# Kernel optimization log

Measured on AMD Instinct MI355X. Metric: run time of the kernel, lower is better.

Reference implementation:

```python
import jax, jax.numpy as jnp
import numpy as np

D = 768; NH = 12; DH = 64; DEPTH = 12; P = 16; IMG = 224; NC = 1000; DFF = 3072
GAMMA = 0.01; MIN_TOKENS = 16; EPS = 1e-6
SCALE = DH ** -0.5
NPATCH = (IMG // P) ** 2  # 196


def _ln(x, w, b, eps=1e-6):
    mu = x.mean(-1, keepdims=True)
    var = ((x - mu) ** 2).mean(-1, keepdims=True)
    return (x - mu) * jax.lax.rsqrt(var + eps) * w + b


def _block(x, p):
    # one pre-norm ViT block; returns new x, attention matrix A [B,H,T,T], values v [B,H,T,DH]
    (l1w, l1b, qw, qb, pw, pb, l2w, l2b, f1w, f1b, f2w, f2b) = p
    B, T, _ = x.shape
    qkv = _ln(x, l1w, l1b) @ qw + qb                      # [B,T,3D]
    qkv = qkv.reshape(B, T, 3, NH, DH).transpose(2, 0, 3, 1, 4)
    q, k, v = qkv[0], qkv[1], qkv[2]                      # [B,H,T,DH]
    A = jax.nn.softmax(jnp.einsum('bhtd,bhsd->bhts', q, k) * SCALE, axis=-1)
    out = jnp.einsum('bhts,bhsd->bhtd', A, v).transpose(0, 2, 1, 3).reshape(B, T, NH * DH)
    x = x + out @ pw + pb
    h = jax.nn.gelu(_ln(x, l2w, l2b) @ f1w + f1b, approximate=False)
    x = x + h @ f2w + f2b
    return x, A, v


def _embed(x, patch_w, patch_b, cls_token, pos_embed):
    B = x.shape[0]
    feat = jax.lax.conv_general_dilated(x, patch_w, (P, P), 'VALID',
                                        dimension_numbers=('NCHW', 'OIHW', 'NCHW'))  # [B,D,14,14]
    feat = feat.reshape(B, D, -1).transpose(0, 2, 1) + patch_b                       # [B,196,D]
    cls = jnp.broadcast_to(cls_token, (B, 1, D))
    return jnp.concatenate([cls, feat], axis=1) + pos_embed                          # [B,197,D]


def setup_inputs() -> dict:
    key = jax.random.key(0)
    ks = jax.random.split(key, 12)
    s = 0.02
    n = lambda k, shape: jax.random.normal(k, shape, jnp.float32) * s
    return {
        'x': jax.random.normal(ks[0], (32, 3, IMG, IMG), jnp.float32),
        'patch_w': n(ks[1], (D, 3, P, P)),
        'patch_b': jnp.zeros((D,), jnp.float32),
        'cls_token': n(ks[2], (1, 1, D)),
        'pos_embed': n(ks[3], (1, NPATCH + 1, D)),
        'ln1_w': jnp.ones((DEPTH, D), jnp.float32),
        'ln1_b': jnp.zeros((DEPTH, D), jnp.float32),
        'qkv_w': n(ks[4], (DEPTH, D, 3 * D)),
        'qkv_b': jnp.zeros((DEPTH, 3 * D), jnp.float32),
        'proj_w': n(ks[5], (DEPTH, D, D)),
        'proj_b': jnp.zeros((DEPTH, D), jnp.float32),
        'ln2_w': jnp.ones((DEPTH, D), jnp.float32),
        'ln2_b': jnp.zeros((DEPTH, D), jnp.float32),
        'fc1_w': n(ks[6], (DEPTH, D, DFF)),
        'fc1_b': jnp.zeros((DEPTH, DFF), jnp.float32),
        'fc2_w': n(ks[7], (DEPTH, DFF, D)),
        'fc2_b': jnp.zeros((DEPTH, D), jnp.float32),
        'norm_w': jnp.ones((D,), jnp.float32),
        'norm_b': jnp.zeros((D,), jnp.float32),
        'head_w': n(ks[8], (D, NC)),
        'head_b': jnp.zeros((NC,), jnp.float32),
    }


def reference(x, patch_w, patch_b, cls_token, pos_embed, ln1_w, ln1_b, qkv_w, qkv_b,
              proj_w, proj_b, ln2_w, ln2_b, fc1_w, fc1_b, fc2_w, fc2_b,
              norm_w, norm_b, head_w, head_b):
    # NOTE: token pruning produces data-dependent shapes, so this runs eagerly
    # (Python control flow on concrete values), exactly mirroring the torch code.
    x = _embed(x, patch_w, patch_b, cls_token, pos_embed)
    N = x.shape[1] - 1
    prev_mass = None
    for l in range(DEPTH):
        p = (ln1_w[l], ln1_b[l], qkv_w[l], qkv_b[l], proj_w[l], proj_b[l],
             ln2_w[l], ln2_b[l], fc1_w[l], fc1_b[l], fc2_w[l], fc2_b[l])
        x, A, v = _block(x, p)
        if N <= MIN_TOKENS:
            continue
        Am = A.mean(axis=1)                                   # [B,T,T] head-mean attention
        Vm = v.mean(axis=1)                                   # [B,T,DH] head-mean values
        rho = (1.0 + Am[:, 0, 0] * jnp.linalg.norm(Vm[:, 0], axis=-1)).mean()
        A_cls = Am[:, 0, 1:N + 1]                             # [B,N] cls->patch attention
        V_pt = Vm[:, 1:N + 1]
        Vc = V_pt - V_pt.mean(axis=1, keepdims=True)
        Vn = jnp.linalg.norm(Vc, axis=-1)                     # [B,N]
        mu = Vn.mean(axis=1, keepdims=True)
        sd = Vn.std(axis=1, keepdims=True, ddof=1)            # torch.std is unbiased
        J = A_cls * jax.nn.relu((Vn - mu) / (sd + EPS))       # [B,N] Jacobian score
        mass = J.sum(axis=1).mean()
        if prev_mass is not None:
            eta = mass / (prev_mass + EPS)
            keep_ratio = jnp.clip(rho * eta, 0.25, 4.0) ** (-GAMMA)
            N_next = max(MIN_TOKENS, int(N * float(keep_ratio)))
        else:
            N_next = N
        if N_next < N:
            idx = jnp.sort(jax.lax.top_k(J.mean(axis=0), N_next)[1]) + 1
            keep = jnp.concatenate([jnp.zeros((1,), idx.dtype), idx])
            x = x[:, keep]
            N = N_next
        prev_mass = mass
    x = _ln(x, norm_w, norm_b)
    return x[:, 0] @ head_w + head_b
```

## Files before the change

kernel.cpp:

```cpp
#include <hip/hip_runtime.h>
#include <math.h>

#define D 768
#define NH 12
#define DH 64
#define DEPTH 12
#define TMAX 197
#define NPATCH 196
#define BATCH 32
#define DFF 3072
#define NC 1000
#define QSTRIDE 2304
#define SCALE 0.125f
#define EPSF 1e-6f

typedef __bf16 bf16x8 __attribute__((ext_vector_type(8)));
typedef float f32x4 __attribute__((ext_vector_type(4)));
typedef short sshort8 __attribute__((ext_vector_type(8)));


__device__ __forceinline__ short f2bf(float x) {
  unsigned u = __float_as_uint(x);
  u = u + 0x7fffu + ((u >> 16) & 1u);
  return (short)(u >> 16);
}
__device__ __forceinline__ float bf2f(short h) {
  return __uint_as_float(((unsigned)(unsigned short)h) << 16);
}
__device__ __forceinline__ void bsplit(float x, short* hp, short* lp) {
  short h = f2bf(x);
  *hp = h;
  *lp = f2bf(x - bf2f(h));
}

__device__ __forceinline__ void gll16(const void* g, void* l) {
  __builtin_amdgcn_global_load_lds(
      (const __attribute__((address_space(1))) void*)g,
      (__attribute__((address_space(3))) void*)l, 16, 0, 0);
}


__device__ __forceinline__ float block_reduce_sum(float v, float* red, int tid) {
  red[tid] = v; __syncthreads();
  #pragma unroll
  for (int o = 128; o > 0; o >>= 1) { if (tid < o) red[tid] += red[tid + o]; __syncthreads(); }
  float r = red[0]; __syncthreads();
  return r;
}

__global__ void fail_kernel(float* out) { out[0] = 1.0e6f; }

__global__ void init_kernel(int* si, float* sf) {
  si[0] = TMAX;
  si[1] = 0;
  si[2] = 0;
  sf[0] = 0.f;
}

__global__ void wsplit_t(const float* __restrict__ W, short* __restrict__ Wpk,
                         int K, int N) {
  __shared__ float t[32][33];
  int n0 = blockIdx.x * 32, k0 = blockIdx.y * 32;
  int tid = threadIdx.x;
  int kk = tid >> 3, n4 = (tid & 7) * 4;
  float4 v = *(const float4*)(W + (size_t)(k0 + kk) * N + n0 + n4);
  t[kk][n4] = v.x; t[kk][n4 + 1] = v.y; t[kk][n4 + 2] = v.z; t[kk][n4 + 3] = v.w;
  __syncthreads();
  int nn = tid >> 3, k4 = (tid & 7) * 4;
  short* dh = Wpk + (size_t)(n0 + nn) * 2 * K + k0 + k4;
  short* dl = dh + K;
  #pragma unroll
  for (int c = 0; c < 4; ++c) bsplit(t[k4 + c][nn], &dh[c], &dl[c]);
}

__global__ void wsplit_nt(const float* __restrict__ W, short* __restrict__ Wpk, int K) {
  const float* src = W + (size_t)blockIdx.x * K;
  short* dh = Wpk + (size_t)blockIdx.x * 2 * K;
  short* dl = dh + K;
  for (int k = threadIdx.x; k < K; k += 256) bsplit(src[k], &dh[k], &dl[k]);
}


__global__ void im2col_kernel(const float* __restrict__ x, short* __restrict__ Impk) {
  int p = blockIdx.x, b = blockIdx.y;
  int py = p / 14, px = p % 14;
  short* dst = Impk + ((size_t)b * NPATCH + p) * 1536;
  for (int k = threadIdx.x; k < D; k += 256) {
    int c = k >> 8; int rem = k & 255; int i = rem >> 4; int j = rem & 15;
    float v = x[(((size_t)b * 3 + c) * 224 + py * 16 + i) * 224 + px * 16 + j];
    bsplit(v, &dst[k], &dst[768 + k]);
  }
}

__global__ void assemble_kernel(const float* __restrict__ PE, const float* __restrict__ cls,
                                const float* __restrict__ pos, float* __restrict__ X) {
  int t = blockIdx.x, b = blockIdx.y; int tid = threadIdx.x;
  float* xp = X + ((size_t)(b * TMAX) + t) * D;
  for (int k = tid; k < D; k += 256) {
    float v = (t == 0) ? cls[k] : PE[((size_t)(b * NPATCH) + (t - 1)) * D + k];
    xp[k] = v + pos[(size_t)t * D + k];
  }
}


__global__ void ln_kernel(const float* __restrict__ Xin, short* __restrict__ XNpk,
                          const float* __restrict__ wgt, const float* __restrict__ bsh,
                          const int* __restrict__ si) {
  int row = blockIdx.x;
  if ((row % TMAX) >= si[0]) return;
  __shared__ float red[256];
  int tid = threadIdx.x;
  const float* xp = Xin + (size_t)row * D;
  float v0 = xp[tid], v1 = xp[tid + 256], v2 = xp[tid + 512];
  float mu = block_reduce_sum(v0 + v1 + v2, red, tid) * (1.0f / 768.0f);
  float d0 = v0 - mu, d1 = v1 - mu, d2 = v2 - mu;
  float var = block_reduce_sum(d0 * d0 + d1 * d1 + d2 * d2, red, tid) * (1.0f / 768.0f);
  float inv = 1.0f / sqrtf(var + EPSF);
  short* op = XNpk + (size_t)row * 1536;
  float y0 = d0 * inv * wgt[tid] + bsh[tid];
  float y1 = d1 * inv * wgt[tid + 256] + bsh[tid + 256];
  float y2 = d2 * inv * wgt[tid + 512] + bsh[tid + 512];
  bsplit(y0, &op[tid], &op[768 + tid]);
  bsplit(y1, &op[tid + 256], &op[768 + tid + 256]);
  bsplit(y2, &op[tid + 512], &op[768 + tid + 512]);
}

__global__ void lnfinal_kernel(const float* __restrict__ X, float* __restrict__ CLSb,
                               const float* __restrict__ wgt, const float* __restrict__ bsh) {
  int b = blockIdx.x; int tid = threadIdx.x;
  __shared__ float red[256];
  const float* xp = X + (size_t)b * TMAX * D;
  float v0 = xp[tid], v1 = xp[tid + 256], v2 = xp[tid + 512];
  float mu = block_reduce_sum(v0 + v1 + v2, red, tid) * (1.0f / 768.0f);
  float d0 = v0 - mu, d1 = v1 - mu, d2 = v2 - mu;
  float var = block_reduce_sum(d0 * d0 + d1 * d1 + d2 * d2, red, tid) * (1.0f / 768.0f);
  float inv = 1.0f / sqrtf(var + EPSF);
  float* op = CLSb + (size_t)b * D;
  op[tid]       = d0 * inv * wgt[tid]       + bsh[tid];
  op[tid + 256] = d1 * inv * wgt[tid + 256] + bsh[tid + 256];
  op[tid + 512] = d2 * inv * wgt[tid + 512] + bsh[tid + 512];
}


#define GTM 128
#define GTN 128
#define GTK 32

template<int EPI>
__global__ __launch_bounds__(256)
void mgemm_kernel(const short* __restrict__ Apk, const short* __restrict__ Bpk,
                  const float* __restrict__ bias, const float* __restrict__ Rsrc,
                  float* __restrict__ Cf, short* __restrict__ Cpk,
                  int M, int K, int N) {
  __shared__ char lds[65536];
  const int tid = threadIdx.x;
  const int ln = tid & 63;
  const int wv = tid >> 6;
  const int wm = wv >> 1, wn = wv & 1;
  const int m0 = blockIdx.y * GTM, n0 = blockIdx.x * GTN;
  const int lm = ln & 15, kc = ln >> 4;
  const size_t rs = 2 * (size_t)K;

  f32x4 acc[4][4];
  f32x4 zv = {0.f, 0.f, 0.f, 0.f};
  #pragma unroll
  for (int i = 0; i < 4; ++i)
    #pragma unroll
    for (int j = 0; j < 4; ++j) acc[i][j] = zv;

  auto stage = [&](int k0, int buf) {
    char* base = lds + (buf << 15);
    #pragma unroll
    for (int i = 0; i < 4; ++i) {
      int s = (i << 8) + tid;
      int r = s >> 3;
      int sl = (s & 7) ^ (r & 7);
      size_t eoff = (size_t)(sl >> 2) * K + (size_t)(k0 + ((sl & 3) << 3));
      int ldsoff = ((i << 8) + (tid & 192)) << 4;
      gll16(Apk + (size_t)(m0 + r) * rs + eoff, base + ldsoff);
      gll16(Bpk + (size_t)(n0 + r) * rs + eoff, base + 16384 + ldsoff);
    }
  };

  const int nk = K / GTK;
  stage(0, 0);
  for (int kt = 0; kt < nk; ++kt) {
    __syncthreads();
    if (kt + 1 < nk) stage((kt + 1) * GTK, (kt + 1) & 1);
    const char* pa = lds + ((kt & 1) << 15);
    const char* pb = pa + 16384;
    bf16x8 bh[4], bl[4];
    #pragma unroll
    for (int j = 0; j < 4; ++j) {
      int c = wn * 64 + j * 16 + lm;
      int bo = c * 128 + ((kc ^ (c & 7)) << 4);
      bh[j] = *(const bf16x8*)(pb + bo);
      bl[j] = *(const bf16x8*)(pb + (bo ^ 64));
    }
    #pragma unroll
    for (int i = 0; i < 4; ++i) {
      int r = wm * 64 + i * 16 + lm;
      int ao = r * 128 + ((kc ^ (r & 7)) << 4);
      bf16x8 ah = *(const bf16x8*)(pa + ao);
      bf16x8 al = *(const bf16x8*)(pa + (ao ^ 64));
      #pragma unroll
      for (int j = 0; j < 4; ++j) {
        acc[i][j] = __builtin_amdgcn_mfma_f32_16x16x32_bf16(ah, bh[j], acc[i][j], 0, 0, 0);
        acc[i][j] = __builtin_amdgcn_mfma_f32_16x16x32_bf16(ah, bl[j], acc[i][j], 0, 0, 0);
        acc[i][j] = __builtin_amdgcn_mfma_f32_16x16x32_bf16(al, bh[j], acc[i][j], 0, 0, 0);
      }
    }
  }

  #pragma unroll
  for (int i = 0; i < 4; ++i) {
    #pragma unroll
    for (int t = 0; t < 4; ++t) {
      int m = m0 + wm * 64 + i * 16 + kc * 4 + t;
      if (m >= M) continue;
      #pragma unroll
      for (int j = 0; j < 4; ++j) {
        int n = n0 + wn * 64 + j * 16 + lm;
        float v = acc[i][j][t] + bias[n];
        if (EPI == 1) v += Rsrc[(size_t)m * N + n];
        if (EPI == 2) {
          v = v * 0.5f * (1.0f + erff(v * 0.70710678118654752f));
          short h = f2bf(v);
          Cpk[(size_t)m * 2 * N + n] = h;
          Cpk[(size_t)m * 2 * N + N + n] = f2bf(v - bf2f(h));
        } else {
          Cf[(size_t)m * N + n] = v;
        }
      }
    }
  }
}


#define BM 128
#define BN 64
#define BK 16

__global__ __launch_bounds__(256, 2)
void gemm_kernel(const float* __restrict__ A, const float* __restrict__ Bw,
                 const float* __restrict__ bias, float* __restrict__ C,
                 int M, int K, int N) {
  __shared__ float As[BK][BM + 4];
  __shared__ float Bs[BK][BN];
  int tid = threadIdx.x;
  int tx = tid & 15;
  int ty = tid >> 4;
  int m0 = blockIdx.y * BM;
  int n0 = blockIdx.x * BN;
  float acc[8][4];
  #pragma unroll
  for (int i = 0; i < 8; ++i)
    #pragma unroll
    for (int j = 0; j < 4; ++j) acc[i][j] = 0.f;
  const int lkA = tid & 15;
  const int lmA = tid >> 4;
  const int lnB = tid & 63;
  const int lkB = tid >> 6;
  for (int k0 = 0; k0 < K; k0 += BK) {
    #pragma unroll
    for (int r = 0; r < 8; ++r) {
      int ml = r * 16 + lmA;
      int m = m0 + ml;
      float va = 0.f;
      if (m < M) va = A[(size_t)m * K + k0 + lkA];
      As[lkA][ml] = va;
    }
    #pragma unroll
    for (int r = 0; r < 4; ++r) {
      int kk = r * 4 + lkB;
      int n = n0 + lnB;
      float vb = 0.f;
      if (n < N) vb = Bw[(size_t)(k0 + kk) * N + n];
      Bs[kk][lnB] = vb;
    }
    __syncthreads();
    #pragma unroll
    for (int kk = 0; kk < BK; ++kk) {
      const float4 b4 = *(const float4*)(&Bs[kk][tx * 4]);
      const float4 a0 = *(const float4*)(&As[kk][ty * 8]);
      const float4 a1 = *(const float4*)(&As[kk][ty * 8 + 4]);
      const float a[8] = {a0.x, a0.y, a0.z, a0.w, a1.x, a1.y, a1.z, a1.w};
      const float bb[4] = {b4.x, b4.y, b4.z, b4.w};
      #pragma unroll
      for (int i = 0; i < 8; ++i)
        #pragma unroll
        for (int j = 0; j < 4; ++j)
          acc[i][j] = fmaf(a[i], bb[j], acc[i][j]);
    }
    __syncthreads();
  }
  #pragma unroll
  for (int i = 0; i < 8; ++i) {
    int m = m0 + ty * 8 + i;
    if (m >= M) continue;
    #pragma unroll
    for (int j = 0; j < 4; ++j) {
      int n = n0 + tx * 4 + j;
      if (n >= N) continue;
      C[(size_t)m * N + n] = acc[i][j] + bias[n];
    }
  }
}


#define QT 64
#define KVT 64

__global__ __launch_bounds__(256)
void mattn_kernel(const float* __restrict__ QKV, short* __restrict__ AOpk,
                  const int* __restrict__ si) {
  const int tok = si[0];
  const int bh = blockIdx.x; const int b = bh / NH, h = bh % NH;
  const int q0 = blockIdx.y * QT;
  if (q0 >= tok) return;
  __shared__ short Kh[4096], Kl[4096], Vth[4096], Vtl[4096];
  __shared__ short Pb[8192];
  const int tid = threadIdx.x;
  const int l = tid & 63, w = tid >> 6;
  const int lm = l & 15, lg = l >> 4;

  bf16x8 qh[2], ql[2];
  {
    int qrow = q0 + w * 16 + lm;
    if (qrow >= TMAX) qrow = TMAX - 1;
    const float* qp = QKV + (size_t)(b * TMAX + qrow) * QSTRIDE + h * DH + lg * 8;
    #pragma unroll
    for (int c = 0; c < 2; ++c) {
      sshort8 hs, ls;
      #pragma unroll
      for (int j = 0; j < 8; ++j) {
        float v = qp[c * 32 + j];
        short hh = f2bf(v);
        hs[j] = hh;
        ls[j] = f2bf(v - bf2f(hh));
      }
      qh[c] = __builtin_bit_cast(bf16x8, hs);
      ql[c] = __builtin_bit_cast(bf16x8, ls);
    }
  }

  float mrun[4], lrun[4];
  f32x4 oacc[4];
  f32x4 zv = {0.f, 0.f, 0.f, 0.f};
  #pragma unroll
  for (int t = 0; t < 4; ++t) { mrun[t] = -1e30f; lrun[t] = 0.f; }
  #pragma unroll
  for (int j = 0; j < 4; ++j) oacc[j] = zv;

  const int r0 = (tid >> 4) * 4;
  const int td4 = (tid & 15) * 4;

  for (int j0 = 0; j0 < tok; j0 += KVT) {
    {
      float vbuf[16];
      #pragma unroll
      for (int i = 0; i < 4; ++i) {
        int gr = j0 + r0 + i; if (gr >= TMAX) gr = TMAX - 1;
        const float* kp = QKV + (size_t)(b * TMAX + gr) * QSTRIDE + D + h * DH + td4;
        float4 kv = *(const float4*)kp;
        short4 sh, sl;
        sh.x = f2bf(kv.x); sl.x = f2bf(kv.x - bf2f(sh.x));
        sh.y = f2bf(kv.y); sl.y = f2bf(kv.y - bf2f(sh.y));
        sh.z = f2bf(kv.z); sl.z = f2bf(kv.z - bf2f(sh.z));
        sh.w = f2bf(kv.w); sl.w = f2bf(kv.w - bf2f(sh.w));
        int r = r0 + i;
        int so = r * 64 + (((td4 >> 3) ^ (r & 7)) << 3) + (td4 & 7);
        *(short4*)(Kh + so) = sh;
        *(short4*)(Kl + so) = sl;
        const float* vp = QKV + (size_t)(b * TMAX + gr) * QSTRIDE + 2 * D + h * DH + td4;
        float4 vv = *(const float4*)vp;
        vbuf[i * 4 + 0] = vv.x; vbuf[i * 4 + 1] = vv.y;
        vbuf[i * 4 + 2] = vv.z; vbuf[i * 4 + 3] = vv.w;
      }
      #pragma unroll
      for (int dd = 0; dd < 4; ++dd) {
        int d = td4 + dd;
        short4 sh, sl;
        float c0 = vbuf[dd], c1 = vbuf[4 + dd], c2 = vbuf[8 + dd], c3 = vbuf[12 + dd];
        sh.x = f2bf(c0); sl.x = f2bf(c0 - bf2f(sh.x));
        sh.y = f2bf(c1); sl.y = f2bf(c1 - bf2f(sh.y));
        sh.z = f2bf(c2); sl.z = f2bf(c2 - bf2f(sh.z));
        sh.w = f2bf(c3); sl.w = f2bf(c3 - bf2f(sh.w));
        int so = d * 64 + (((r0 >> 3) ^ (d & 7)) << 3) + (r0 & 7);
        *(short4*)(Vth + so) = sh;
        *(short4*)(Vtl + so) = sl;
      }
    }
    __syncthreads();

    f32x4 sacc[4];
    #pragma unroll
    for (int jk = 0; jk < 4; ++jk) sacc[jk] = zv;
    #pragma unroll
    for (int c = 0; c < 2; ++c) {
      #pragma unroll
      for (int jk = 0; jk < 4; ++jk) {
        int row = jk * 16 + lm;
        int so = row * 64 + (((c * 4 + lg) ^ (row & 7)) << 3);
        bf16x8 kbh = *(const bf16x8*)(Kh + so);
        bf16x8 kbl = *(const bf16x8*)(Kl + so);
        sacc[jk] = __builtin_amdgcn_mfma_f32_16x16x32_bf16(qh[c], kbh, sacc[jk], 0, 0, 0);
        sacc[jk] = __builtin_amdgcn_mfma_f32_16x16x32_bf16(qh[c], kbl, sacc[jk], 0, 0, 0);
        sacc[jk] = __builtin_amdgcn_mfma_f32_16x16x32_bf16(ql[c], kbh, sacc[jk], 0, 0, 0);
      }
    }

    float p[4][4];
    #pragma unroll
    for (int jk = 0; jk < 4; ++jk) {
      bool valid = (j0 + jk * 16 + lm) < tok;
      #pragma unroll
      for (int t = 0; t < 4; ++t)
        p[jk][t] = valid ? sacc[jk][t] * SCALE : -1e30f;
    }
    float mt[4], mnew[4], co[4], rs[4];
    #pragma unroll
    for (int t = 0; t < 4; ++t) {
      mt[t] = fmaxf(fmaxf(p[0][t], p[1][t]), fmaxf(p[2][t], p[3][t]));
      #pragma unroll
      for (int off = 1; off < 16; off <<= 1)
        mt[t] = fmaxf(mt[t], __shfl_xor(mt[t], off, 16));
      mnew[t] = fmaxf(mrun[t], mt[t]);
      co[t] = expf(mrun[t] - mnew[t]);
      rs[t] = 0.f;
    }
    #pragma unroll
    for (int jk = 0; jk < 4; ++jk)
      #pragma unroll
      for (int t = 0; t < 4; ++t) {
        p[jk][t] = expf(p[jk][t] - mnew[t]);
        rs[t] += p[jk][t];
      }
    #pragma unroll
    for (int t = 0; t < 4; ++t) {
      #pragma unroll
      for (int off = 1; off < 16; off <<= 1)
        rs[t] += __shfl_xor(rs[t], off, 16);
      lrun[t] = lrun[t] * co[t] + rs[t];
      mrun[t] = mnew[t];
    }
    #pragma unroll
    for (int jd = 0; jd < 4; ++jd)
      #pragma unroll
      for (int t = 0; t < 4; ++t) oacc[jd][t] *= co[t];

    short* Pw = Pb + w * 2048;
    #pragma unroll
    for (int jk = 0; jk < 4; ++jk)
      #pragma unroll
      for (int t = 0; t < 4; ++t) {
        int q = lg * 4 + t;
        int col = jk * 16 + lm;
        short hh = f2bf(p[jk][t]);
        short hl = f2bf(p[jk][t] - bf2f(hh));
        int so = q * 64 + (((col >> 3) ^ (q & 7)) << 3) + (col & 7);
        Pw[so] = hh;
        Pw[1024 + so] = hl;
      }

    #pragma unroll
    for (int c = 0; c < 2; ++c) {
      int aro = lm * 64 + (((c * 4 + lg) ^ (lm & 7)) << 3);
      bf16x8 pah = *(const bf16x8*)(Pw + aro);
      bf16x8 pal = *(const bf16x8*)(Pw + 1024 + aro);
      #pragma unroll
      for (int jd = 0; jd < 4; ++jd) {
        int d = jd * 16 + lm;
        int so = d * 64 + (((c * 4 + lg) ^ (d & 7)) << 3);
        bf16x8 vbh = *(const bf16x8*)(Vth + so);
        bf16x8 vbl = *(const bf16x8*)(Vtl + so);
        oacc[jd] = __builtin_amdgcn_mfma_f32_16x16x32_bf16(pah, vbh, oacc[jd], 0, 0, 0);
        oacc[jd] = __builtin_amdgcn_mfma_f32_16x16x32_bf16(pah, vbl, oacc[jd], 0, 0, 0);
        oacc[jd] = __builtin_amdgcn_mfma_f32_16x16x32_bf16(pal, vbh, oacc[jd], 0, 0, 0);
      }
    }
    __syncthreads();
  }

  #pragma unroll
  for (int t = 0; t < 4; ++t) {
    int q = q0 + w * 16 + lg * 4 + t;
    if (q >= tok) continue;
    float inv = 1.0f / lrun[t];
    short* op = AOpk + (size_t)(b * TMAX + q) * 1536 + h * DH;
    #pragma unroll
    for (int jd = 0; jd < 4; ++jd) {
      int d = jd * 16 + lm;
      float y = oacc[jd][t] * inv;
      short hh = f2bf(y);
      op[d] = hh;
      op[768 + d] = f2bf(y - bf2f(hh));
    }
  }
}

__global__ void clsrow_kernel(const float* __restrict__ QKV, float* __restrict__ Pcls,
                              const int* __restrict__ si) {
  int tok = si[0];
  int bh = blockIdx.x; int b = bh / NH, h = bh % NH;
  int tid = threadIdx.x;
  __shared__ float q[DH];
  __shared__ float red[256];
  if (tid < DH) q[tid] = QKV[((size_t)(b * TMAX)) * QSTRIDE + h * DH + tid];
  __syncthreads();
  float sval = -1e30f;
  if (tid < tok) {
    const float* kp = QKV + ((size_t)(b * TMAX) + tid) * QSTRIDE + D + h * DH;
    float a = 0.f;
    #pragma unroll
    for (int dd = 0; dd < DH; ++dd) a = fmaf(q[dd], kp[dd], a);
    sval = a * SCALE;
  }
  red[tid] = sval; __syncthreads();
  #pragma unroll
  for (int o = 128; o > 0; o >>= 1) { if (tid < o) red[tid] = fmaxf(red[tid], red[tid + o]); __syncthreads(); }
  float mx = red[0]; __syncthreads();
  float e = (tid < tok) ? expf(sval - mx) : 0.f;
  red[tid] = e; __syncthreads();
  #pragma unroll
  for (int o = 128; o > 0; o >>= 1) { if (tid < o) red[tid] += red[tid + o]; __syncthreads(); }
  if (tid < tok) Pcls[(size_t)bh * TMAX + tid] = e / red[0];
}

__global__ void aclsmean_kernel(const float* __restrict__ Pcls, float* __restrict__ Acls,
                                const int* __restrict__ si) {
  int tok = si[0]; int b = blockIdx.x; int tid = threadIdx.x;
  if (tid < tok) {
    float s = 0.f;
    #pragma unroll
    for (int h = 0; h < NH; ++h) s += Pcls[((size_t)b * NH + h) * TMAX + tid];
    Acls[b * TMAX + tid] = s * (1.0f / 12.0f);
  }
}

__global__ void vmean_kernel(const float* __restrict__ QKV, float* __restrict__ Vm,
                             const int* __restrict__ si) {
  int tok = si[0];
  int t = blockIdx.x, b = blockIdx.y;
  if (t >= tok) return;
  int d = threadIdx.x;
  const float* vp = QKV + ((size_t)(b * TMAX + t)) * QSTRIDE + 2 * D;
  float s = 0.f;
  #pragma unroll
  for (int h = 0; h < NH; ++h) s += vp[h * DH + d];
  Vm[((size_t)b * TMAX + t) * DH + d] = s * (1.0f / 12.0f);
}


__global__ void stats_kernel(const float* __restrict__ Vm, const float* __restrict__ Acls,
                             float* __restrict__ Jbuf, float* __restrict__ Jsum,
                             float* __restrict__ rhot, const int* __restrict__ si) {
  int tok = si[0]; int N = tok - 1;
  if (N <= 16) return;
  int b = blockIdx.x; int tid = threadIdx.x;
  __shared__ float red[256];
  __shared__ float vmean[DH];
  __shared__ float Vn[NPATCH];
  const float* vb = Vm + (size_t)b * TMAX * DH;

  float x0 = 0.f;
  if (tid < DH) { float v = vb[tid]; x0 = v * v; }
  red[tid] = x0; __syncthreads();
  #pragma unroll
  for (int o = 128; o > 0; o >>= 1) { if (tid < o) red[tid] += red[tid + o]; __syncthreads(); }
  if (tid == 0) rhot[b] = 1.0f + Acls[b * TMAX] * sqrtf(red[0]);
  __syncthreads();

  int d = tid & 63, part = tid >> 6;
  float s = 0.f;
  for (int t = 1 + part; t <= N; t += 4) s += vb[(size_t)t * DH + d];
  red[tid] = s; __syncthreads();
  if (tid < DH) vmean[tid] = (red[tid] + red[tid + 64] + red[tid + 128] + red[tid + 192]) / (float)N;
  __syncthreads();

  if (tid < N) {
    const float* vp = vb + (size_t)(tid + 1) * DH;
    float a = 0.f;
    #pragma unroll
    for (int dd = 0; dd < DH; ++dd) { float z = vp[dd] - vmean[dd]; a = fmaf(z, z, a); }
    Vn[tid] = sqrtf(a);
  }
  __syncthreads();

  red[tid] = (tid < N) ? Vn[tid] : 0.f; __syncthreads();
  #pragma unroll
  for (int o = 128; o > 0; o >>= 1) { if (tid < o) red[tid] += red[tid + o]; __syncthreads(); }
  float mu = red[0] / (float)N;
  __syncthreads();
  float dv = (tid < N) ? (Vn[tid] - mu) : 0.f;
  red[tid] = dv * dv; __syncthreads();
  #pragma unroll
  for (int o = 128; o > 0; o >>= 1) { if (tid < o) red[tid] += red[tid + o]; __syncthreads(); }
  float sd = sqrtf(red[0] / (float)(N - 1));
  __syncthreads();

  float Jv = 0.f;
  if (tid < N) {
    float z = (Vn[tid] - mu) / (sd + EPSF);
    z = fmaxf(z, 0.f);
    Jv = Acls[b * TMAX + 1 + tid] * z;
    Jbuf[b * NPATCH + tid] = Jv;
  }
  red[tid] = Jv; __syncthreads();
  #pragma unroll
  for (int o = 128; o > 0; o >>= 1) { if (tid < o) red[tid] += red[tid + o]; __syncthreads(); }
  if (tid == 0) Jsum[b] = red[0];
}

__global__ void decide_kernel(const float* __restrict__ Jbuf, const float* __restrict__ Jsum,
                              const float* __restrict__ rhot, int* __restrict__ keep,
                              int* __restrict__ si, float* __restrict__ sf) {
  int tok = si[0]; int N = tok - 1;
  int tid = threadIdx.x;
  if (N <= 16) { if (tid == 0) si[2] = 0; return; }
  __shared__ float red[256];
  __shared__ float Jms[NPATCH];
  __shared__ int sel[NPATCH];

  red[tid] = (tid < BATCH) ? rhot[tid] : 0.f; __syncthreads();
  #pragma unroll
  for (int o = 128; o > 0; o >>= 1) { if (tid < o) red[tid] += red[tid + o]; __syncthreads(); }
  float rho = red[0] / (float)BATCH; __syncthreads();
  red[tid] = (tid < BATCH) ? Jsum[tid] : 0.f; __syncthreads();
  #pragma unroll
  for (int o = 128; o > 0; o >>= 1) { if (tid < o) red[tid] += red[tid + o]; __syncthreads(); }
  float mass = red[0] / (float)BATCH;
  int prev_valid = si[1];
  float prev = sf[0];
  __syncthreads();

  int N_next = N;
  if (prev_valid) {
    float eta = mass / (prev + EPSF);
    float re = rho * eta;
    re = fminf(fmaxf(re, 0.25f), 4.0f);
    double kr = pow((double)re, -0.01);
    int nn = (int)((double)N * kr);
    N_next = nn > 16 ? nn : 16;
  }
  if (tid == 0) { si[1] = 1; sf[0] = mass; }

  if (N_next < N) {
    if (tid < N) {
      float sJ = 0.f;
      for (int bb = 0; bb < BATCH; ++bb) sJ += Jbuf[bb * NPATCH + tid];
      Jms[tid] = sJ / (float)BATCH;
    }
    __syncthreads();
    if (tid < N) {
      float me = Jms[tid]; int rank = 0;
      for (int s2 = 0; s2 < N; ++s2) {
        float ov = Jms[s2];
        if (ov > me || (ov == me && s2 < tid)) ++rank;
      }
      sel[tid] = (rank < N_next) ? 1 : 0;
    }
    __syncthreads();
    if (tid == 0) {
      int c = 0; keep[c++] = 0;
      for (int t2 = 0; t2 < N; ++t2) if (sel[t2]) keep[c++] = t2 + 1;
      si[0] = N_next + 1;
      si[2] = 1;
    }
  } else {
    if (tid == 0) si[2] = 0;
  }
}

__global__ void gather_kernel(const float* __restrict__ X, float* __restrict__ T,
                              const int* __restrict__ keep, const int* __restrict__ si) {
  if (!si[2]) return;
  int tok = si[0];
  int i = blockIdx.x, b = blockIdx.y;
  if (i >= tok) return;
  int src = keep[i];
  const float* xp = X + ((size_t)(b * TMAX) + src) * D;
  float* tp = T + ((size_t)(b * TMAX) + i) * D;
  int tid = threadIdx.x;
  tp[tid] = xp[tid]; tp[tid + 256] = xp[tid + 256]; tp[tid + 512] = xp[tid + 512];
}

__global__ void copyback_kernel(const float* __restrict__ T, float* __restrict__ X,
                                const int* __restrict__ si) {
  if (!si[2]) return;
  int tok = si[0];
  int i = blockIdx.x, b = blockIdx.y;
  if (i >= tok) return;
  const float* tp = T + ((size_t)(b * TMAX) + i) * D;
  float* xp = X + ((size_t)(b * TMAX) + i) * D;
  int tid = threadIdx.x;
  xp[tid] = tp[tid]; xp[tid + 256] = tp[tid + 256]; xp[tid + 512] = tp[tid + 512];
}


extern "C" void kernel_launch(void* const* d_in, const int* in_sizes, int n_in,
                              void* d_out, int out_size, void* d_ws, size_t ws_size,
                              hipStream_t stream) {
  (void)in_sizes; (void)n_in; (void)out_size;
  const float* x       = (const float*)d_in[0];
  const float* patch_w = (const float*)d_in[1];
  const float* patch_b = (const float*)d_in[2];
  const float* cls_tok = (const float*)d_in[3];
  const float* pos     = (const float*)d_in[4];
  const float* ln1w    = (const float*)d_in[5];
  const float* ln1b    = (const float*)d_in[6];
  const float* qkvw    = (const float*)d_in[7];
  const float* qkvb    = (const float*)d_in[8];
  const float* projw   = (const float*)d_in[9];
  const float* projb   = (const float*)d_in[10];
  const float* ln2w    = (const float*)d_in[11];
  const float* ln2b    = (const float*)d_in[12];
  const float* fc1w    = (const float*)d_in[13];
  const float* fc1b    = (const float*)d_in[14];
  const float* fc2w    = (const float*)d_in[15];
  const float* fc2b    = (const float*)d_in[16];
  const float* normw   = (const float*)d_in[17];
  const float* normb   = (const float*)d_in[18];
  const float* headw   = (const float*)d_in[19];
  const float* headb   = (const float*)d_in[20];
  float* out = (float*)d_out;

  char* w = (char*)d_ws;
  size_t off = 0;
  auto alloc = [&](size_t bytes) -> void* {
    void* p = w + off;
    off += (bytes + 255) & ~(size_t)255;
    return p;
  };
  const size_t MROWS = (size_t)BATCH * TMAX;
  float* X    = (float*)alloc(MROWS * D * 4);
  short* XNpk = (short*)alloc(MROWS * 1536 * 2);
  float* QKV  = (float*)alloc(MROWS * QSTRIDE * 4);
  short* AOpk = (short*)alloc(MROWS * 1536 * 2);
  short* Hpk  = (short*)alloc(MROWS * 2 * DFF * 2);
  float* Vm   = (float*)alloc(MROWS * DH * 4);
  float* Pcls = (float*)alloc((size_t)BATCH * NH * TMAX * 4);
  float* Acls = (float*)alloc((size_t)BATCH * TMAX * 4);
  float* Jbuf = (float*)alloc((size_t)BATCH * NPATCH * 4);
  float* Jsum = (float*)alloc(BATCH * 4);
  float* rhot = (float*)alloc(BATCH * 4);
  int*   keep = (int*)alloc(256 * 4);
  int*   si   = (int*)alloc(64 * 4);
  float* sf   = (float*)alloc(64 * 4);
  float* CLS  = (float*)alloc((size_t)BATCH * D * 4);
  short* Wq   = (short*)alloc((size_t)QSTRIDE * 2 * D * 2);
  short* Wp   = (short*)alloc((size_t)D * 2 * D * 2);
  short* W1   = (short*)alloc((size_t)DFF * 2 * D * 2);
  short* W2   = (short*)alloc((size_t)D * 2 * DFF * 2);
  short* Wpat = (short*)alloc((size_t)D * 2 * D * 2);
  short* Impk = Hpk;
  float* TMP  = (float*)Hpk;
  float* Ef32 = QKV;

  if (off > ws_size) {
    fail_kernel<<<1, 1, 0, stream>>>(out);
    return;
  }

  init_kernel<<<1, 1, 0, stream>>>(si, sf);

  im2col_kernel<<<dim3(NPATCH, BATCH), 256, 0, stream>>>(x, Impk);
  wsplit_nt<<<D, 256, 0, stream>>>(patch_w, Wpat, D);
  mgemm_kernel<0><<<dim3(D / GTN, (BATCH * NPATCH + GTM - 1) / GTM), 256, 0, stream>>>(
      Impk, Wpat, patch_b, nullptr, Ef32, nullptr, BATCH * NPATCH, D, D);
  assemble_kernel<<<dim3(TMAX, BATCH), 256, 0, stream>>>(Ef32, cls_tok, pos, X);

  const int MG = (int)((MROWS + GTM - 1) / GTM);

  for (int l = 0; l < DEPTH; ++l) {
    const float* l1w = ln1w + l * D;
    const float* l1b = ln1b + l * D;
    const float* qw  = qkvw + (size_t)l * D * 3 * D;
    const float* qb  = qkvb + (size_t)l * 3 * D;
    const float* pw  = projw + (size_t)l * D * D;
    const float* pb  = projb + (size_t)l * D;
    const float* l2w = ln2w + l * D;
    const float* l2b = ln2b + l * D;
    const float* f1w = fc1w + (size_t)l * D * DFF;
    const float* f1b = fc1b + (size_t)l * DFF;
    const float* f2w = fc2w + (size_t)l * DFF * D;
    const float* f2b = fc2b + (size_t)l * D;

    wsplit_t<<<dim3(QSTRIDE / 32, D / 32), 256, 0, stream>>>(qw, Wq, D, QSTRIDE);
    wsplit_t<<<dim3(D / 32, D / 32), 256, 0, stream>>>(pw, Wp, D, D);
    wsplit_t<<<dim3(DFF / 32, D / 32), 256, 0, stream>>>(f1w, W1, D, DFF);
    wsplit_t<<<dim3(D / 32, DFF / 32), 256, 0, stream>>>(f2w, W2, DFF, D);

    ln_kernel<<<BATCH * TMAX, 256, 0, stream>>>(X, XNpk, l1w, l1b, si);
    mgemm_kernel<0><<<dim3(QSTRIDE / GTN, MG), 256, 0, stream>>>(
        XNpk, Wq, qb, nullptr, QKV, nullptr, (int)MROWS, D, QSTRIDE);
    mattn_kernel<<<dim3(BATCH * NH, (TMAX + QT - 1) / QT), 256, 0, stream>>>(QKV, AOpk, si);
    clsrow_kernel<<<BATCH * NH, 256, 0, stream>>>(QKV, Pcls, si);
    aclsmean_kernel<<<BATCH, 256, 0, stream>>>(Pcls, Acls, si);
    vmean_kernel<<<dim3(TMAX, BATCH), 64, 0, stream>>>(QKV, Vm, si);
    mgemm_kernel<1><<<dim3(D / GTN, MG), 256, 0, stream>>>(
        AOpk, Wp, pb, X, X, nullptr, (int)MROWS, D, D);
    ln_kernel<<<BATCH * TMAX, 256, 0, stream>>>(X, XNpk, l2w, l2b, si);
    mgemm_kernel<2><<<dim3(DFF / GTN, MG), 256, 0, stream>>>(
        XNpk, W1, f1b, nullptr, nullptr, Hpk, (int)MROWS, D, DFF);
    mgemm_kernel<1><<<dim3(D / GTN, MG), 256, 0, stream>>>(
        Hpk, W2, f2b, X, X, nullptr, (int)MROWS, DFF, D);
    stats_kernel<<<BATCH, 256, 0, stream>>>(Vm, Acls, Jbuf, Jsum, rhot, si);
    decide_kernel<<<1, 256, 0, stream>>>(Jbuf, Jsum, rhot, keep, si, sf);
    gather_kernel<<<dim3(TMAX, BATCH), 256, 0, stream>>>(X, TMP, keep, si);
    copyback_kernel<<<dim3(TMAX, BATCH), 256, 0, stream>>>(TMP, X, si);
  }

  lnfinal_kernel<<<BATCH, 256, 0, stream>>>(X, CLS, normw, normb);
  gemm_kernel<<<dim3(16, 1), 256, 0, stream>>>(CLS, headw, headb, out, BATCH, D, NC);
}
```

Before: 6.481 ms.

## Stage GEMM tiles through registers with single LDS buffer and swizzled block order

The GEMM kernel drops the double-buffered direct global-to-LDS loads. It now prefetches the next K-tile into registers while computing from a single 32KB LDS buffer, which halves LDS use so that three blocks can fit per CU (launch_bounds 256,3). The grid is flattened to 1D with an optional swizzle that groups blocks by XCD chunks and N-column strips, aiming for better L2 reuse. The cost is an extra register footprint and a barrier per K-step, since LDS writes and reads now share one buffer.

```diff
diff --git a/kernel.cpp b/kernel.cpp
--- a/kernel.cpp
+++ b/kernel.cpp
@@ -31,12 +31,6 @@
   short h = f2bf(x);
   *hp = h;
   *lp = f2bf(x - bf2f(h));
-}
-
-__device__ __forceinline__ void gll16(const void* g, void* l) {
-  __builtin_amdgcn_global_load_lds(
-      (const __attribute__((address_space(1))) void*)g,
-      (__attribute__((address_space(3))) void*)l, 16, 0, 0);
 }
 
 
@@ -146,18 +140,35 @@
 #define GTN 128
 #define GTK 32
 
-template<int EPI>
-__global__ __launch_bounds__(256)
+template<int EPI, int SWZ>
+__global__ __launch_bounds__(256, 3)
 void mgemm_kernel(const short* __restrict__ Apk, const short* __restrict__ Bpk,
                   const float* __restrict__ bias, const float* __restrict__ Rsrc,
                   float* __restrict__ Cf, short* __restrict__ Cpk,
-                  int M, int K, int N) {
-  __shared__ char lds[65536];
+                  int M, int K, int N, int nx, int ny, int wsub) {
+  __shared__ char lds[32768];
   const int tid = threadIdx.x;
   const int ln = tid & 63;
   const int wv = tid >> 6;
   const int wm = wv >> 1, wn = wv & 1;
-  const int m0 = blockIdx.y * GTM, n0 = blockIdx.x * GTN;
+
+  int bx, by;
+  if (SWZ) {
+    int d = blockIdx.x;
+    int q = ny >> 3, r = ny & 7;
+    int rows, m0, l;
+    int big = (q + 1) * nx;
+    if (d < r * big) { int c = d / big; l = d - c * big; rows = q + 1; m0 = c * (q + 1); }
+    else { int d2 = d - r * big; int sm = q * nx; int c2 = d2 / sm; l = d2 - c2 * sm; rows = q; m0 = r * (q + 1) + c2 * q; }
+    int wspan = wsub * rows;
+    int j = l / wspan; int t = l - j * wspan;
+    int ml = t / wsub; int dx = t - ml * wsub;
+    bx = j * wsub + dx; by = m0 + ml;
+  } else {
+    bx = blockIdx.x % nx; by = blockIdx.x / nx;
+  }
+
+  const int m0 = by * GTM, n0 = bx * GTN;
   const int lm = ln & 15, kc = ln >> 4;
   const size_t rs = 2 * (size_t)K;
 
@@ -168,27 +179,40 @@
     #pragma unroll
     for (int j = 0; j < 4; ++j) acc[i][j] = zv;
 
-  auto stage = [&](int k0, int buf) {
-    char* base = lds + (buf << 15);
+  float4 ar[4], br[4];
+  auto load_regs = [&](int k0) {
     #pragma unroll
     for (int i = 0; i < 4; ++i) {
       int s = (i << 8) + tid;
-      int r = s >> 3;
-      int sl = (s & 7) ^ (r & 7);
-      size_t eoff = (size_t)(sl >> 2) * K + (size_t)(k0 + ((sl & 3) << 3));
-      int ldsoff = ((i << 8) + (tid & 192)) << 4;
-      gll16(Apk + (size_t)(m0 + r) * rs + eoff, base + ldsoff);
-      gll16(Bpk + (size_t)(n0 + r) * rs + eoff, base + 16384 + ldsoff);
+      int r = s >> 3; int ls = s & 7;
+      size_t eoff = (size_t)(ls >> 2) * K + (size_t)(k0 + ((ls & 3) << 3));
+      ar[i] = *(const float4*)(Apk + (size_t)(m0 + r) * rs + eoff);
+      br[i] = *(const float4*)(Bpk + (size_t)(n0 + r) * rs + eoff);
     }
   };
+  auto write_lds = [&]() {
+    #pragma unroll
+    for (int i = 0; i < 4; ++i) {
+      int s = (i << 8) + tid;
+      int r = s >> 3; int ls = s & 7;
+      int off = (r << 7) + ((ls ^ (r & 7)) << 4);
+      *(float4*)(lds + off) = ar[i];
+      *(float4*)(lds + 16384 + off) = br[i];
+    }
+  };
 
   const int nk = K / GTK;
-  stage(0, 0);
+  load_regs(0);
   for (int kt = 0; kt < nk; ++kt) {
     __syncthreads();
-    if (kt + 1 < nk) stage((kt + 1) * GTK, (kt + 1) & 1);
-    const char* pa = lds + ((kt & 1) << 15);
-    const char* pb = pa + 16384;
+    write_lds();
+    if (kt + 1 < nk) load_regs((kt + 1) * GTK);
+    asm volatile("s_waitcnt lgkmcnt(0)" ::: "memory");
+    __builtin_amdgcn_s_barrier();
+    __builtin_amdgcn_sched_barrier(0);
+
+    const char* pa = lds;
+    const char* pb = lds + 16384;
     bf16x8 bh[4], bl[4];
     #pragma unroll
     for (int j = 0; j < 4; ++j) {
@@ -766,11 +790,9 @@
 
   im2col_kernel<<<dim3(NPATCH, BATCH), 256, 0, stream>>>(x, Impk);
   wsplit_nt<<<D, 256, 0, stream>>>(patch_w, Wpat, D);
-  mgemm_kernel<0><<<dim3(D / GTN, (BATCH * NPATCH + GTM - 1) / GTM), 256, 0, stream>>>(
-      Impk, Wpat, patch_b, nullptr, Ef32, nullptr, BATCH * NPATCH, D, D);
+  mgemm_kernel<0, 1><<<6 * 49, 256, 0, stream>>>(
+      Impk, Wpat, patch_b, nullptr, Ef32, nullptr, BATCH * NPATCH, D, D, 6, 49, 6);
   assemble_kernel<<<dim3(TMAX, BATCH), 256, 0, stream>>>(Ef32, cls_tok, pos, X);
-
-  const int MG = (int)((MROWS + GTM - 1) / GTM);
 
   for (int l = 0; l < DEPTH; ++l) {
     const float* l1w = ln1w + l * D;
@@ -792,19 +814,19 @@
     wsplit_t<<<dim3(D / 32, DFF / 32), 256, 0, stream>>>(f2w, W2, DFF, D);
 
     ln_kernel<<<BATCH * TMAX, 256, 0, stream>>>(X, XNpk, l1w, l1b, si);
-    mgemm_kernel<0><<<dim3(QSTRIDE / GTN, MG), 256, 0, stream>>>(
-        XNpk, Wq, qb, nullptr, QKV, nullptr, (int)MROWS, D, QSTRIDE);
+    mgemm_kernel<0, 1><<<18 * 50, 256, 0, stream>>>(
+        XNpk, Wq, qb, nullptr, QKV, nullptr, (int)MROWS, D, QSTRIDE, 18, 50, 6);
     mattn_kernel<<<dim3(BATCH * NH, (TMAX + QT - 1) / QT), 256, 0, stream>>>(QKV, AOpk, si);
     clsrow_kernel<<<BATCH * NH, 256, 0, stream>>>(QKV, Pcls, si);
     aclsmean_kernel<<<BATCH, 256, 0, stream>>>(Pcls, Acls, si);
     vmean_kernel<<<dim3(TMAX, BATCH), 64, 0, stream>>>(QKV, Vm, si);
-    mgemm_kernel<1><<<dim3(D / GTN, MG), 256, 0, stream>>>(
-        AOpk, Wp, pb, X, X, nullptr, (int)MROWS, D, D);
+    mgemm_kernel<1, 1><<<6 * 50, 256, 0, stream>>>(
+        AOpk, Wp, pb, X, X, nullptr, (int)MROWS, D, D, 6, 50, 6);
     ln_kernel<<<BATCH * TMAX, 256, 0, stream>>>(X, XNpk, l2w, l2b, si);
-    mgemm_kernel<2><<<dim3(DFF / GTN, MG), 256, 0, stream>>>(
-        XNpk, W1, f1b, nullptr, nullptr, Hpk, (int)MROWS, D, DFF);
-    mgemm_kernel<1><<<dim3(D / GTN, MG), 256, 0, stream>>>(
-        Hpk, W2, f2b, X, X, nullptr, (int)MROWS, DFF, D);
+    mgemm_kernel<2, 1><<<24 * 50, 256, 0, stream>>>(
+        XNpk, W1, f1b, nullptr, nullptr, Hpk, (int)MROWS, D, DFF, 24, 50, 8);
+    mgemm_kernel<1, 0><<<6 * 50, 256, 0, stream>>>(
+        Hpk, W2, f2b, X, X, nullptr, (int)MROWS, DFF, D, 6, 50, 6);
     stats_kernel<<<BATCH, 256, 0, stream>>>(Vm, Acls, Jbuf, Jsum, rhot, si);
     decide_kernel<<<1, 256, 0, stream>>>(Jbuf, Jsum, rhot, keep, si, sf);
     gather_kernel<<<dim3(TMAX, BATCH), 256, 0, stream>>>(X, TMP, keep, si);
```

New measurement: 18.31 ms. +182.6%, slower.
